# Kernel optimization log

Measured on AMD Instinct MI355X. Metric: run time of the kernel, lower is better.

## Reference

```python
import jax, jax.numpy as jnp
import numpy as np

B, S, D = 2, 2048, 2048
NH, NKV = 32, 8
HD = D // NH          # 64
NREP = NH // NKV      # 4


def _rope(x, cos, sin):
    # x: [B, S, H, HD]; cos/sin: [S, HD//2]
    x2 = x.reshape(*x.shape[:-1], HD // 2, 2)
    x0, x1 = x2[..., 0], x2[..., 1]
    c = cos[None, :, None, :]
    s = sin[None, :, None, :]
    r0 = x0 * c - x1 * s
    r1 = x0 * s + x1 * c
    return jnp.stack([r0, r1], axis=-1).reshape(x.shape)


def setup_inputs() -> dict:
    key = jax.random.key(0)
    ks = jax.random.split(key, 5)
    x = jax.random.normal(ks[0], (B, S, D), dtype=jnp.float32)
    wq = jax.random.normal(ks[1], (D, NH * HD), dtype=jnp.float32) * (D ** -0.5)
    wk = jax.random.normal(ks[2], (D, NKV * HD), dtype=jnp.float32) * (D ** -0.5)
    wv = jax.random.normal(ks[3], (D, NKV * HD), dtype=jnp.float32) * (D ** -0.5)
    wo = jax.random.normal(ks[4], (NH * HD, D), dtype=jnp.float32) * (D ** -0.5)
    # standard RoPE frequencies: theta = 10000^(-2i/HD)
    inv_freq = 1.0 / (10000.0 ** (np.arange(0, HD, 2, dtype=np.float32) / HD))
    angles = np.arange(S, dtype=np.float32)[:, None] * inv_freq[None, :]  # [S, HD/2]
    freqs_cos = jnp.asarray(np.cos(angles))
    freqs_sin = jnp.asarray(np.sin(angles))
    return {"x": x, "freqs_cos": freqs_cos, "freqs_sin": freqs_sin,
            "wq": wq, "wk": wk, "wv": wv, "wo": wo}


def reference(x, freqs_cos, freqs_sin, wq, wk, wv, wo):
    b, s, _ = x.shape
    xq = (x @ wq).reshape(b, s, NH, HD)
    xk = (x @ wk).reshape(b, s, NKV, HD)
    xv = (x @ wv).reshape(b, s, NKV, HD)
    xq = _rope(xq, freqs_cos, freqs_sin)
    xk = _rope(xk, freqs_cos, freqs_sin)
    # GQA repeat_kv: expand kv heads to NH
    keys = jnp.repeat(xk, NREP, axis=2)    # [B, S, NH, HD]
    values = jnp.repeat(xv, NREP, axis=2)
    scores = jnp.einsum('bqhd,bkhd->bhqk', xq, keys) / jnp.sqrt(jnp.float32(HD))
    causal = jnp.tril(jnp.ones((s, s), dtype=bool))
    scores = jnp.where(causal[None, None], scores, -jnp.inf)
    attn = jax.nn.softmax(scores.astype(jnp.float32), axis=-1).astype(xq.dtype)
    out = jnp.einsum('bhqk,bkhd->bqhd', attn, values).reshape(b, s, NH * HD)
    return out @ wo
```

## Files before the change

kernel.cpp:

```cpp
#include <hip/hip_runtime.h>
#include <hip/hip_bf16.h>

#define S_LEN 2048
#define DMODEL 2048
#define N_H 32
#define N_KV 8
#define H_D 64
#define ROWS 4096
#define QKV_LD 3072

typedef __bf16 bf16x8 __attribute__((ext_vector_type(8)));
typedef float f32x4 __attribute__((ext_vector_type(4)));

static __device__ __forceinline__ unsigned short f2bf(float f) {
  unsigned int u = __float_as_uint(f);
  u += 0x7FFFu + ((u >> 16) & 1u);
  return (unsigned short)(u >> 16);
}
static __device__ __forceinline__ unsigned short f2bf_tr(float f) {
  return (unsigned short)(__float_as_uint(f) >> 16);
}
static __device__ __forceinline__ float bf2f(unsigned short s) {
  return __uint_as_float((unsigned int)s << 16);
}

static __device__ __forceinline__ void async16(const void* g, void* l) {
  __builtin_amdgcn_global_load_lds(
      (const __attribute__((address_space(1))) unsigned int*)g,
      (__attribute__((address_space(3))) unsigned int*)l, 16, 0, 0);
}

__global__ __launch_bounds__(256) void cvt_bf16_k(
    const float* __restrict__ in, unsigned short* __restrict__ out) {
  const size_t i = ((size_t)blockIdx.x * 256 + threadIdx.x) * 8;
  const float4 a = *(const float4*)&in[i];
  const float4 b = *(const float4*)&in[i + 4];
  union { unsigned short u[8]; uint4 v; } p;
  p.u[0] = f2bf(a.x); p.u[1] = f2bf(a.y); p.u[2] = f2bf(a.z); p.u[3] = f2bf(a.w);
  p.u[4] = f2bf(b.x); p.u[5] = f2bf(b.y); p.u[6] = f2bf(b.z); p.u[7] = f2bf(b.w);
  *(uint4*)&out[i] = p.v;
}

__global__ __launch_bounds__(256) void prep_all_k(
    const float* __restrict__ x, const float* __restrict__ wq,
    const float* __restrict__ wk, const float* __restrict__ wv,
    const float* __restrict__ wo, unsigned short* __restrict__ xb,
    unsigned short* __restrict__ wqkvT, unsigned short* __restrict__ woT) {
  const int z = blockIdx.z;
  if (z == 4) {
    const size_t i =
        (((size_t)blockIdx.y * 64 + blockIdx.x) * 256 + threadIdx.x) * 8;
    const float4 a = *(const float4*)&x[i];
    const float4 b = *(const float4*)&x[i + 4];
    union { unsigned short u[8]; uint4 v; } p;
    p.u[0] = f2bf(a.x); p.u[1] = f2bf(a.y); p.u[2] = f2bf(a.z); p.u[3] = f2bf(a.w);
    p.u[4] = f2bf(b.x); p.u[5] = f2bf(b.y); p.u[6] = f2bf(b.z); p.u[7] = f2bf(b.w);
    *(uint4*)&xb[i] = p.v;
    return;
  }
  const float* in;
  unsigned short* out;
  int C;
  if (z == 0)      { in = wq; out = wqkvT;                  C = 2048; }
  else if (z == 1) { in = wk; out = wqkvT + 2048ull * 2048; C = 512;  }
  else if (z == 2) { in = wv; out = wqkvT + 2560ull * 2048; C = 512;  }
  else             { in = wo; out = woT;                    C = 2048; }
  if (blockIdx.x * 32 >= C) return;

  __shared__ unsigned short tile[32][33];
  const int tx = threadIdx.x & 31;
  const int ty = threadIdx.x >> 5;
  const int r0 = blockIdx.y * 32;
  const int c0 = blockIdx.x * 32;
#pragma unroll
  for (int i = 0; i < 32; i += 8)
    tile[ty + i][tx] = f2bf(in[(size_t)(r0 + ty + i) * C + c0 + tx]);
  __syncthreads();
#pragma unroll
  for (int i = 0; i < 32; i += 8)
    out[(size_t)(c0 + ty + i) * 2048 + r0 + tx] = tile[tx][ty + i];
}

#define SCALE_LOG2E 0.18033688011112042f

__global__ __launch_bounds__(256) void rope_vt_k(
    unsigned short* __restrict__ qkv, unsigned short* __restrict__ vT,
    const float* __restrict__ fc, const float* __restrict__ fs) {
  const int blk = blockIdx.x;
  if (blk < 20480) {
    const int PQ = ROWS * N_H * (H_D / 2);
    const int PK = ROWS * N_KV * (H_D / 2);
    const int idx = blk * 256 + threadIdx.x;
    if (idx >= PQ + PK) return;
    unsigned short* base;
    float c, sn;
    bool isq;
    if (idx < PQ) {
      const int i = idx & 31;
      const int h = (idx >> 5) & 31;
      const int row = idx >> 10;
      const int s = row & (S_LEN - 1);
      c = fc[s * 32 + i];
      sn = fs[s * 32 + i];
      base = qkv + (size_t)row * QKV_LD + h * H_D + 2 * i;
      isq = true;
    } else {
      const int p = idx - PQ;
      const int i = p & 31;
      const int h = (p >> 5) & 7;
      const int row = p >> 8;
      const int s = row & (S_LEN - 1);
      c = fc[s * 32 + i];
      sn = fs[s * 32 + i];
      base = qkv + (size_t)row * QKV_LD + 2048 + h * H_D + 2 * i;
      isq = false;
    }
    const float x0 = bf2f(base[0]);
    const float x1 = bf2f(base[1]);
    const float sc = isq ? SCALE_LOG2E : 1.0f;
    base[0] = f2bf((x0 * c - x1 * sn) * sc);
    base[1] = f2bf((x0 * sn + x1 * c) * sc);
  } else {
    __shared__ unsigned short tile[32][33];
    const int t = blk - 20480;
    const int bx = t & 15;
    const int by = t >> 4;
    const unsigned short* in = qkv + 2560;
    const int tx = threadIdx.x & 31;
    const int ty = threadIdx.x >> 5;
    const int r0 = by * 32;
    const int c0 = bx * 32;
#pragma unroll
    for (int i = 0; i < 32; i += 8)
      tile[ty + i][tx] = in[(size_t)(r0 + ty + i) * QKV_LD + c0 + tx];
    __syncthreads();
#pragma unroll
    for (int i = 0; i < 32; i += 8)
      vT[(size_t)(c0 + ty + i) * ROWS + r0 + tx] = tile[tx][ty + i];
  }
}

template <int STORE_BF16>
__global__ __launch_bounds__(256) void gemm_bt_k(
    const unsigned short* __restrict__ A, const unsigned short* __restrict__ BT,
    void* __restrict__ Cp, int M, int N, int K, int lda) {
  __shared__ __align__(16) unsigned short As[128 * 32];
  __shared__ __align__(16) unsigned short Bs[128 * 32];
  const int tid = threadIdx.x;
  const int wave = tid >> 6;
  const int lane = tid & 63;
  const int quad = lane >> 4;
  const int l16 = lane & 15;
  const int m0 = blockIdx.x * 128;
  const int n0 = blockIdx.y * 128;
  const int wm = (wave >> 1) * 64;
  const int wn = (wave & 1) * 64;
  const int rsub = lane >> 2;
  const int coff = (lane & 3) * 8;
  f32x4 acc[4][4] = {};

  for (int kt = 0; kt < K; kt += 32) {
    __syncthreads();
#pragma unroll
    for (int t = 0; t < 2; t++) {
      const int row = wave * 32 + t * 16 + rsub;
      async16(&A[(size_t)(m0 + row) * lda + kt + coff],
              &As[(wave * 32 + t * 16) * 32]);
      async16(&BT[(size_t)(n0 + row) * K + kt + coff],
              &Bs[(wave * 32 + t * 16) * 32]);
    }
    __syncthreads();
    bf16x8 af[4], bfr[4];
#pragma unroll
    for (int i = 0; i < 4; i++)
      af[i] = *(const bf16x8*)&As[(wm + i * 16 + l16) * 32 + quad * 8];
#pragma unroll
    for (int j = 0; j < 4; j++)
      bfr[j] = *(const bf16x8*)&Bs[(wn + j * 16 + l16) * 32 + quad * 8];
#pragma unroll
    for (int i = 0; i < 4; i++)
#pragma unroll
      for (int j = 0; j < 4; j++)
        acc[i][j] =
            __builtin_amdgcn_mfma_f32_16x16x32_bf16(af[i], bfr[j], acc[i][j], 0, 0, 0);
  }

#pragma unroll
  for (int i = 0; i < 4; i++) {
#pragma unroll
    for (int e = 0; e < 4; e++) {
      const int mrow = m0 + wm + i * 16 + quad * 4 + e;
#pragma unroll
      for (int j = 0; j < 4; j++) {
        const int ncol = n0 + wn + j * 16 + l16;
        const float val = acc[i][j][e];
        if (STORE_BF16) {
          ((unsigned short*)Cp)[(size_t)mrow * N + ncol] = f2bf(val);
        } else {
          ((float*)Cp)[(size_t)mrow * N + ncol] = val;
        }
      }
    }
  }
}

template <int AF32, int STORE_BF16>
__global__ __launch_bounds__(256) void gemm_k(
    const void* __restrict__ Ap, const float* __restrict__ B,
    void* __restrict__ Cp, int M, int N, int K) {
  constexpr int LDP = 40;
  __shared__ __align__(16) unsigned short As[128 * LDP];
  __shared__ __align__(16) unsigned short Bs[128 * LDP];
  const int tid = threadIdx.x;
  const int wave = tid >> 6;
  const int lane = tid & 63;
  const int quad = lane >> 4;
  const int l16 = lane & 15;
  const int m0 = blockIdx.x * 128;
  const int n0 = blockIdx.y * 128;
  const int wm = (wave >> 1) * 64;
  const int wn = (wave & 1) * 64;
  f32x4 acc[4][4] = {};

  for (int kt = 0; kt < K; kt += 32) {
    __syncthreads();
    if (AF32) {
      const float* A = (const float*)Ap;
      for (int c = tid; c < 1024; c += 256) {
        const int r = c >> 3;
        const int cc = (c & 7) << 2;
        const float4 w = *(const float4*)&A[(size_t)(m0 + r) * K + kt + cc];
        union { unsigned short u[4]; uint2 v; } p;
        p.u[0] = f2bf(w.x); p.u[1] = f2bf(w.y);
        p.u[2] = f2bf(w.z); p.u[3] = f2bf(w.w);
        *(uint2*)&As[r * LDP + cc] = p.v;
      }
    } else {
      const unsigned short* A = (const unsigned short*)Ap;
      for (int c = tid; c < 512; c += 256) {
        const int r = c >> 2;
        const int cc = (c & 3) << 3;
        *(uint4*)&As[r * LDP + cc] =
            *(const uint4*)&A[(size_t)(m0 + r) * K + kt + cc];
      }
    }
    for (int c = tid; c < 1024; c += 256) {
      const int kr = c >> 5;
      const int nc = (c & 31) << 2;
      const float4 w = *(const float4*)&B[(size_t)(kt + kr) * N + n0 + nc];
      Bs[(nc + 0) * LDP + kr] = f2bf(w.x);
      Bs[(nc + 1) * LDP + kr] = f2bf(w.y);
      Bs[(nc + 2) * LDP + kr] = f2bf(w.z);
      Bs[(nc + 3) * LDP + kr] = f2bf(w.w);
    }
    __syncthreads();
    bf16x8 af[4], bfr[4];
#pragma unroll
    for (int i = 0; i < 4; i++)
      af[i] = *(const bf16x8*)&As[(wm + i * 16 + l16) * LDP + quad * 8];
#pragma unroll
    for (int j = 0; j < 4; j++)
      bfr[j] = *(const bf16x8*)&Bs[(wn + j * 16 + l16) * LDP + quad * 8];
#pragma unroll
    for (int i = 0; i < 4; i++)
#pragma unroll
      for (int j = 0; j < 4; j++)
        acc[i][j] =
            __builtin_amdgcn_mfma_f32_16x16x32_bf16(af[i], bfr[j], acc[i][j], 0, 0, 0);
  }
#pragma unroll
  for (int i = 0; i < 4; i++) {
#pragma unroll
    for (int e = 0; e < 4; e++) {
      const int mrow = m0 + wm + i * 16 + quad * 4 + e;
#pragma unroll
      for (int j = 0; j < 4; j++) {
        const int ncol = n0 + wn + j * 16 + l16;
        const float val = acc[i][j][e];
        if (STORE_BF16) {
          ((unsigned short*)Cp)[(size_t)mrow * N + ncol] = f2bf(val);
        } else {
          ((float*)Cp)[(size_t)mrow * N + ncol] = val;
        }
      }
    }
  }
}

__global__ __launch_bounds__(256) void rope_k(
    unsigned short* __restrict__ q, unsigned short* __restrict__ kk,
    const float* __restrict__ fc, const float* __restrict__ fs,
    int qstride, int kstride) {
  const int PQ = ROWS * N_H * (H_D / 2);
  const int PK = ROWS * N_KV * (H_D / 2);
  const int idx = blockIdx.x * 256 + threadIdx.x;
  if (idx >= PQ + PK) return;
  unsigned short* base;
  float c, sn;
  if (idx < PQ) {
    const int i = idx & 31;
    const int h = (idx >> 5) & 31;
    const int row = idx >> 10;
    const int s = row & (S_LEN - 1);
    c = fc[s * 32 + i];
    sn = fs[s * 32 + i];
    base = q + (size_t)row * qstride + h * H_D + 2 * i;
  } else {
    const int p = idx - PQ;
    const int i = p & 31;
    const int h = (p >> 5) & 7;
    const int row = p >> 8;
    const int s = row & (S_LEN - 1);
    c = fc[s * 32 + i];
    sn = fs[s * 32 + i];
    base = kk + (size_t)row * kstride + h * H_D + 2 * i;
  }
  const float x0 = bf2f(base[0]);
  const float x1 = bf2f(base[1]);
  base[0] = f2bf(x0 * c - x1 * sn);
  base[1] = f2bf(x0 * sn + x1 * c);
}

#define LK 72

__global__ __launch_bounds__(256) void attn_mfma6_k(
    const unsigned short* __restrict__ qkv, const unsigned short* __restrict__ vT,
    unsigned short* __restrict__ ao) {
  const int pair = blockIdx.x, h = blockIdx.y, b = blockIdx.z;
  const int hk = h >> 2;
  const int tid = threadIdx.x;
  const int wave = tid >> 6;
  const int l16 = tid & 15;
  const int quad = (tid & 63) >> 4;
  const int rr = tid >> 2;
  const int dc = (tid & 3) * 16;

  __shared__ __align__(16) unsigned short Ks[2][64 * LK];
  __shared__ __align__(16) unsigned short Vt[2][64 * LK];
  __shared__ __align__(16) unsigned short Ps[4][32 * LK];

  bf16x8 ones;
#pragma unroll
  for (int j = 0; j < 8; j++) ones[j] = (__bf16)1.0f;

  const size_t kbase =
      (size_t)(b * S_LEN) * QKV_LD + 2048 + hk * H_D + dc;
  const size_t vbase = (size_t)(hk * H_D + rr) * ROWS + b * S_LEN + dc;

  for (int sel = 0; sel < 2; ++sel) {
    const int qb = sel ? (15 - pair) : pair;
    const int row0 = qb * 128;
    const int ktiles = 2 * qb + 2;

    bf16x8 af[2][2];
#pragma unroll
    for (int r = 0; r < 2; r++) {
      const size_t qrow =
          (size_t)(b * S_LEN + row0 + wave * 32 + r * 16 + l16);
#pragma unroll
      for (int c = 0; c < 2; c++)
        af[r][c] =
            *(const bf16x8*)&qkv[qrow * QKV_LD + h * H_D + c * 32 + quad * 8];
    }

    f32x4 o_acc[2][4] = {};
    f32x4 l_acc[2] = {};

    uint4 rk0, rk1, rv0, rv1;
    {
      const size_t kro = kbase + (size_t)rr * QKV_LD;
      rk0 = *(const uint4*)&qkv[kro];
      rk1 = *(const uint4*)&qkv[kro + 8];
      rv0 = *(const uint4*)&vT[vbase];
      rv1 = *(const uint4*)&vT[vbase + 8];
    }
    __syncthreads();
    *(uint4*)&Ks[0][rr * LK + dc] = rk0;
    *(uint4*)&Ks[0][rr * LK + dc + 8] = rk1;
    *(uint4*)&Vt[0][rr * LK + dc] = rv0;
    *(uint4*)&Vt[0][rr * LK + dc + 8] = rv1;

    int cur = 0;
    for (int kt = 0; kt < ktiles; ++kt) {
      if (kt + 1 < ktiles) {
        const size_t kro = kbase + (size_t)((kt + 1) * 64 + rr) * QKV_LD;
        rk0 = *(const uint4*)&qkv[kro];
        rk1 = *(const uint4*)&qkv[kro + 8];
        const size_t vro = vbase + (size_t)(kt + 1) * 64;
        rv0 = *(const uint4*)&vT[vro];
        rv1 = *(const uint4*)&vT[vro + 8];
      }
      __syncthreads();

      f32x4 sacc[2][4];
#pragma unroll
      for (int n = 0; n < 4; n++) {
        f32x4 z0 = {}, z1 = {};
#pragma unroll
        for (int c = 0; c < 2; c++) {
          const bf16x8 bk =
              *(const bf16x8*)&Ks[cur][(n * 16 + l16) * LK + c * 32 + quad * 8];
          z0 = __builtin_amdgcn_mfma_f32_16x16x32_bf16(af[0][c], bk, z0, 0, 0, 0);
          z1 = __builtin_amdgcn_mfma_f32_16x16x32_bf16(af[1][c], bk, z1, 0, 0, 0);
        }
        sacc[0][n] = z0;
        sacc[1][n] = z1;
      }

      const bool maybe_mask = (kt >= 2 * qb);
      const int krel0 = (kt - 2 * qb) * 64;
#pragma unroll
      for (int r = 0; r < 2; r++) {
        const int qrel = wave * 32 + r * 16 + quad * 4;
        if (maybe_mask) {
#pragma unroll
          for (int n = 0; n < 4; n++)
#pragma unroll
            for (int e = 0; e < 4; e++) {
              float pe = exp2f(sacc[r][n][e]);
              if ((krel0 + n * 16 + l16) > (qrel + e)) pe = 0.f;
              Ps[wave][(r * 16 + quad * 4 + e) * LK + n * 16 + l16] =
                  f2bf_tr(pe);
            }
        } else {
#pragma unroll
          for (int n = 0; n < 4; n++)
#pragma unroll
            for (int e = 0; e < 4; e++)
              Ps[wave][(r * 16 + quad * 4 + e) * LK + n * 16 + l16] =
                  f2bf_tr(exp2f(sacc[r][n][e]));
        }
      }

      bf16x8 pf[2][2];
#pragma unroll
      for (int r = 0; r < 2; r++)
#pragma unroll
        for (int c = 0; c < 2; c++)
          pf[r][c] = *(const bf16x8*)&Ps[wave][(r * 16 + l16) * LK + c * 32 +
                                              quad * 8];
#pragma unroll
      for (int c = 0; c < 2; c++) {
        l_acc[0] = __builtin_amdgcn_mfma_f32_16x16x32_bf16(pf[0][c], ones,
                                                           l_acc[0], 0, 0, 0);
        l_acc[1] = __builtin_amdgcn_mfma_f32_16x16x32_bf16(pf[1][c], ones,
                                                           l_acc[1], 0, 0, 0);
      }
#pragma unroll
      for (int n = 0; n < 4; n++)
#pragma unroll
        for (int c = 0; c < 2; c++) {
          const bf16x8 bv =
              *(const bf16x8*)&Vt[cur][(n * 16 + l16) * LK + c * 32 + quad * 8];
          o_acc[0][n] =
              __builtin_amdgcn_mfma_f32_16x16x32_bf16(pf[0][c], bv, o_acc[0][n], 0, 0, 0);
          o_acc[1][n] =
              __builtin_amdgcn_mfma_f32_16x16x32_bf16(pf[1][c], bv, o_acc[1][n], 0, 0, 0);
        }

      if (kt + 1 < ktiles) {
        const int nxt = cur ^ 1;
        *(uint4*)&Ks[nxt][rr * LK + dc] = rk0;
        *(uint4*)&Ks[nxt][rr * LK + dc + 8] = rk1;
        *(uint4*)&Vt[nxt][rr * LK + dc] = rv0;
        *(uint4*)&Vt[nxt][rr * LK + dc + 8] = rv1;
      }
      cur ^= 1;
    }

#pragma unroll
    for (int r = 0; r < 2; r++)
#pragma unroll
      for (int e = 0; e < 4; e++) {
        const float inv = 1.f / l_acc[r][e];
        const size_t row = (size_t)(b * S_LEN + row0 + wave * 32 + r * 16 +
                                    quad * 4 + e);
#pragma unroll
        for (int n = 0; n < 4; n++)
          ao[row * QKV_LD + h * H_D + n * 16 + l16] =
              f2bf(o_acc[r][n][e] * inv);
      }
  }
}

__global__ __launch_bounds__(256) void attn_mfma_k(
    const unsigned short* __restrict__ q, const unsigned short* __restrict__ k,
    const unsigned short* __restrict__ v, unsigned short* __restrict__ ao) {
  const int qt = blockIdx.x, h = blockIdx.y, b = blockIdx.z;
  const int hk = h >> 2;
  const int tid = threadIdx.x;
  const int wave = tid >> 6;
  const int l16 = tid & 15;
  const int quad = (tid & 63) >> 4;

  __shared__ __align__(16) unsigned short Ks[64 * LK];
  __shared__ __align__(16) unsigned short Vt[64 * LK];
  __shared__ __align__(16) unsigned short Ps[64 * LK];

  bf16x8 af[2];
  {
    const size_t qrow = (size_t)(b * S_LEN + qt * 64 + wave * 16 + l16);
#pragma unroll
    for (int c = 0; c < 2; c++)
      af[c] = *(const bf16x8*)&q[qrow * DMODEL + h * H_D + c * 32 + quad * 8];
  }

  f32x4 o_acc[4] = {};
  float m_i[4], l_i[4];
#pragma unroll
  for (int e = 0; e < 4; e++) { m_i[e] = -INFINITY; l_i[e] = 0.f; }

  for (int kt = 0; kt <= qt; ++kt) {
    const int kb = kt * 64;
    __syncthreads();
    {
      const int kr = tid >> 2;
      const int dc = (tid & 3) * 16;
      const size_t gro = (size_t)(b * S_LEN + kb + kr) * (N_KV * H_D) + hk * H_D + dc;
      *(uint4*)&Ks[kr * LK + dc] = *(const uint4*)&k[gro];
      *(uint4*)&Ks[kr * LK + dc + 8] = *(const uint4*)&k[gro + 8];
      union { unsigned short u[8]; uint4 v; } w0, w1;
      w0.v = *(const uint4*)&v[gro];
      w1.v = *(const uint4*)&v[gro + 8];
#pragma unroll
      for (int j = 0; j < 8; j++) Vt[(dc + j) * LK + kr] = w0.u[j];
#pragma unroll
      for (int j = 0; j < 8; j++) Vt[(dc + 8 + j) * LK + kr] = w1.u[j];
    }
    __syncthreads();

    f32x4 sacc[4];
#pragma unroll
    for (int n = 0; n < 4; n++) {
      f32x4 z = {};
#pragma unroll
      for (int c = 0; c < 2; c++) {
        const bf16x8 bk = *(const bf16x8*)&Ks[(n * 16 + l16) * LK + c * 32 + quad * 8];
        z = __builtin_amdgcn_mfma_f32_16x16x32_bf16(af[c], bk, z, 0, 0, 0);
      }
      sacc[n] = z;
    }

    float p[4][4], mnew[4];
#pragma unroll
    for (int e = 0; e < 4; e++) mnew[e] = m_i[e];
#pragma unroll
    for (int n = 0; n < 4; n++)
#pragma unroll
      for (int e = 0; e < 4; e++) {
        float s = sacc[n][e] * 0.125f;
        if (kt == qt && (n * 16 + l16) > (wave * 16 + quad * 4 + e))
          s = -INFINITY;
        p[n][e] = s;
        mnew[e] = fmaxf(mnew[e], s);
      }
#pragma unroll
    for (int e = 0; e < 4; e++) {
      mnew[e] = fmaxf(mnew[e], __shfl_xor(mnew[e], 1));
      mnew[e] = fmaxf(mnew[e], __shfl_xor(mnew[e], 2));
      mnew[e] = fmaxf(mnew[e], __shfl_xor(mnew[e], 4));
      mnew[e] = fmaxf(mnew[e], __shfl_xor(mnew[e], 8));
      const float alpha = __expf(m_i[e] - mnew[e]);
      m_i[e] = mnew[e];
      l_i[e] *= alpha;
#pragma unroll
      for (int n = 0; n < 4; n++) o_acc[n][e] *= alpha;
    }
#pragma unroll
    for (int n = 0; n < 4; n++)
#pragma unroll
      for (int e = 0; e < 4; e++) {
        const float pe = __expf(p[n][e] - m_i[e]);
        p[n][e] = pe;
        l_i[e] += pe;
      }

#pragma unroll
    for (int n = 0; n < 4; n++)
#pragma unroll
      for (int e = 0; e < 4; e++)
        Ps[(wave * 16 + quad * 4 + e) * LK + n * 16 + l16] = f2bf(p[n][e]);
    __syncthreads();

    bf16x8 pf[2];
#pragma unroll
    for (int c = 0; c < 2; c++)
      pf[c] = *(const bf16x8*)&Ps[(wave * 16 + l16) * LK + c * 32 + quad * 8];
#pragma unroll
    for (int n = 0; n < 4; n++)
#pragma unroll
      for (int c = 0; c < 2; c++) {
        const bf16x8 bv = *(const bf16x8*)&Vt[(n * 16 + l16) * LK + c * 32 + quad * 8];
        o_acc[n] = __builtin_amdgcn_mfma_f32_16x16x32_bf16(pf[c], bv, o_acc[n], 0, 0, 0);
      }
  }

#pragma unroll
  for (int e = 0; e < 4; e++) {
    l_i[e] += __shfl_xor(l_i[e], 1);
    l_i[e] += __shfl_xor(l_i[e], 2);
    l_i[e] += __shfl_xor(l_i[e], 4);
    l_i[e] += __shfl_xor(l_i[e], 8);
    const float inv = 1.f / l_i[e];
    const size_t row = (size_t)(b * S_LEN + qt * 64 + wave * 16 + quad * 4 + e);
#pragma unroll
    for (int n = 0; n < 4; n++)
      ao[row * DMODEL + h * H_D + n * 16 + l16] = f2bf(o_acc[n][e] * inv);
  }
}

extern "C" void kernel_launch(void* const* d_in, const int* in_sizes, int n_in,
                              void* d_out, int out_size, void* d_ws, size_t ws_size,
                              hipStream_t stream) {
  const float* x = (const float*)d_in[0];
  const float* fc = (const float*)d_in[1];
  const float* fs = (const float*)d_in[2];
  const float* wq = (const float*)d_in[3];
  const float* wk = (const float*)d_in[4];
  const float* wv = (const float*)d_in[5];
  const float* wo = (const float*)d_in[6];

  char* ws = (char*)d_ws;
  const dim3 b256(256);

  if (ws_size >= (64ull << 20)) {
    unsigned short* qkv = (unsigned short*)(ws);
    unsigned short* xb = (unsigned short*)(ws + (24ull << 20));
    unsigned short* wqkvT = (unsigned short*)(ws + (40ull << 20));
    unsigned short* woT = (unsigned short*)(ws + (52ull << 20));
    unsigned short* vT = (unsigned short*)(ws + (60ull << 20));

    prep_all_k<<<dim3(64, 64, 5), b256, 0, stream>>>(x, wq, wk, wv, wo, xb,
                                                     wqkvT, woT);

    gemm_bt_k<1><<<dim3(32, 24), b256, 0, stream>>>(xb, wqkvT, qkv, 4096, 3072,
                                                    2048, 2048);

    rope_vt_k<<<dim3(20480 + 2048), b256, 0, stream>>>(qkv, vT, fc, fs);

    attn_mfma6_k<<<dim3(8, N_H, 2), b256, 0, stream>>>(qkv, vT, qkv);

    gemm_bt_k<0><<<dim3(32, 16), b256, 0, stream>>>(qkv, woT, d_out, 4096, 2048,
                                                    2048, QKV_LD);
  } else {
    unsigned short* q = (unsigned short*)(ws);
    unsigned short* k = (unsigned short*)(ws + (16ull << 20));
    unsigned short* v = (unsigned short*)(ws + (20ull << 20));
    unsigned short* xb = (unsigned short*)(ws + (24ull << 20));
    const bool have_xb = ws_size >= (40ull << 20);

    if (have_xb) {
      cvt_bf16_k<<<dim3(ROWS * DMODEL / (256 * 8)), b256, 0, stream>>>(x, xb);
      gemm_k<0, 1><<<dim3(32, 16), b256, 0, stream>>>(xb, wq, q, 4096, 2048, 2048);
      gemm_k<0, 1><<<dim3(32, 4), b256, 0, stream>>>(xb, wk, k, 4096, 512, 2048);
      gemm_k<0, 1><<<dim3(32, 4), b256, 0, stream>>>(xb, wv, v, 4096, 512, 2048);
    } else {
      gemm_k<1, 1><<<dim3(32, 16), b256, 0, stream>>>(x, wq, q, 4096, 2048, 2048);
      gemm_k<1, 1><<<dim3(32, 4), b256, 0, stream>>>(x, wk, k, 4096, 512, 2048);
      gemm_k<1, 1><<<dim3(32, 4), b256, 0, stream>>>(x, wv, v, 4096, 512, 2048);
    }

    rope_k<<<dim3(20480), b256, 0, stream>>>(q, k, fc, fs, N_H * H_D, N_KV * H_D);
    attn_mfma_k<<<dim3(S_LEN / 64, N_H, 2), b256, 0, stream>>>(q, k, v, q);
    gemm_k<0, 0><<<dim3(32, 16), b256, 0, stream>>>(q, wo, d_out, 4096, 2048, 2048);
  }
}
```

Baseline: 331.1 us.

## Swizzle attention LDS tiles, swap QK MFMA operands, and launch one block per q-tile

The attention kernel drops padded LDS rows (stride 72) and uses XOR-swizzled 64-wide rows for K, V and P tiles to avoid bank conflicts while cutting shared memory. The QK^T MFMA operands are swapped so each lane holds four consecutive keys of one query row, which lets P be packed into a single 8-byte LDS store per fragment instead of scalar 2-byte stores. The paired causal q-block scheme (two q-tiles per block for load balance) is replaced by one q-tile per block with heaviest tiles first, doubling the grid. This trades the explicit balancing for more blocks, higher occupancy and less per-block serial work.

```diff
diff --git a/kernel.cpp b/kernel.cpp
--- a/kernel.cpp
+++ b/kernel.cpp
@@ -16,9 +16,6 @@
   unsigned int u = __float_as_uint(f);
   u += 0x7FFFu + ((u >> 16) & 1u);
   return (unsigned short)(u >> 16);
-}
-static __device__ __forceinline__ unsigned short f2bf_tr(float f) {
-  return (unsigned short)(__float_as_uint(f) >> 16);
 }
 static __device__ __forceinline__ float bf2f(unsigned short s) {
   return __uint_as_float((unsigned int)s << 16);
@@ -321,12 +318,11 @@
   base[1] = f2bf(x0 * sn + x1 * c);
 }
 
-#define LK 72
-
-__global__ __launch_bounds__(256) void attn_mfma6_k(
+__global__ __launch_bounds__(256) void attn_mfma7_k(
     const unsigned short* __restrict__ qkv, const unsigned short* __restrict__ vT,
     unsigned short* __restrict__ ao) {
-  const int pair = blockIdx.x, h = blockIdx.y, b = blockIdx.z;
+  const int qb = 15 - blockIdx.x;
+  const int h = blockIdx.y, b = blockIdx.z;
   const int hk = h >> 2;
   const int tid = threadIdx.x;
   const int wave = tid >> 6;
@@ -334,154 +330,152 @@
   const int quad = (tid & 63) >> 4;
   const int rr = tid >> 2;
   const int dc = (tid & 3) * 16;
-
-  __shared__ __align__(16) unsigned short Ks[2][64 * LK];
-  __shared__ __align__(16) unsigned short Vt[2][64 * LK];
-  __shared__ __align__(16) unsigned short Ps[4][32 * LK];
+  const int rx = (l16 & 7) << 3;
+  const int sx = (rr & 7) << 3;
+
+  __shared__ __align__(16) unsigned short Ks[2][64 * 64];
+  __shared__ __align__(16) unsigned short Vt[2][64 * 64];
+  __shared__ __align__(16) unsigned short Ps[4][32 * 64];
 
   bf16x8 ones;
 #pragma unroll
   for (int j = 0; j < 8; j++) ones[j] = (__bf16)1.0f;
+
+  const int row0 = qb * 128;
+  const int ktiles = 2 * qb + 2;
+
+  bf16x8 af[2][2];
+#pragma unroll
+  for (int r = 0; r < 2; r++) {
+    const size_t qrow = (size_t)(b * S_LEN + row0 + wave * 32 + r * 16 + l16);
+#pragma unroll
+    for (int c = 0; c < 2; c++)
+      af[r][c] =
+          *(const bf16x8*)&qkv[qrow * QKV_LD + h * H_D + c * 32 + quad * 8];
+  }
+
+  f32x4 o_acc[2][4] = {};
+  f32x4 l_acc[2] = {};
 
   const size_t kbase =
       (size_t)(b * S_LEN) * QKV_LD + 2048 + hk * H_D + dc;
   const size_t vbase = (size_t)(hk * H_D + rr) * ROWS + b * S_LEN + dc;
 
-  for (int sel = 0; sel < 2; ++sel) {
-    const int qb = sel ? (15 - pair) : pair;
-    const int row0 = qb * 128;
-    const int ktiles = 2 * qb + 2;
-
-    bf16x8 af[2][2];
-#pragma unroll
-    for (int r = 0; r < 2; r++) {
-      const size_t qrow =
-          (size_t)(b * S_LEN + row0 + wave * 32 + r * 16 + l16);
-#pragma unroll
-      for (int c = 0; c < 2; c++)
-        af[r][c] =
-            *(const bf16x8*)&qkv[qrow * QKV_LD + h * H_D + c * 32 + quad * 8];
-    }
-
-    f32x4 o_acc[2][4] = {};
-    f32x4 l_acc[2] = {};
-
-    uint4 rk0, rk1, rv0, rv1;
-    {
-      const size_t kro = kbase + (size_t)rr * QKV_LD;
+  uint4 rk0, rk1, rv0, rv1;
+  {
+    const size_t kro = kbase + (size_t)rr * QKV_LD;
+    rk0 = *(const uint4*)&qkv[kro];
+    rk1 = *(const uint4*)&qkv[kro + 8];
+    rv0 = *(const uint4*)&vT[vbase];
+    rv1 = *(const uint4*)&vT[vbase + 8];
+  }
+  *(uint4*)&Ks[0][rr * 64 + (dc ^ sx)] = rk0;
+  *(uint4*)&Ks[0][rr * 64 + ((dc + 8) ^ sx)] = rk1;
+  *(uint4*)&Vt[0][rr * 64 + (dc ^ sx)] = rv0;
+  *(uint4*)&Vt[0][rr * 64 + ((dc + 8) ^ sx)] = rv1;
+
+  int cur = 0;
+  for (int kt = 0; kt < ktiles; ++kt) {
+    if (kt + 1 < ktiles) {
+      const size_t kro = kbase + (size_t)((kt + 1) * 64 + rr) * QKV_LD;
       rk0 = *(const uint4*)&qkv[kro];
       rk1 = *(const uint4*)&qkv[kro + 8];
-      rv0 = *(const uint4*)&vT[vbase];
-      rv1 = *(const uint4*)&vT[vbase + 8];
-    }
-    __syncthreads();
-    *(uint4*)&Ks[0][rr * LK + dc] = rk0;
-    *(uint4*)&Ks[0][rr * LK + dc + 8] = rk1;
-    *(uint4*)&Vt[0][rr * LK + dc] = rv0;
-    *(uint4*)&Vt[0][rr * LK + dc + 8] = rv1;
-
-    int cur = 0;
-    for (int kt = 0; kt < ktiles; ++kt) {
-      if (kt + 1 < ktiles) {
-        const size_t kro = kbase + (size_t)((kt + 1) * 64 + rr) * QKV_LD;
-        rk0 = *(const uint4*)&qkv[kro];
-        rk1 = *(const uint4*)&qkv[kro + 8];
-        const size_t vro = vbase + (size_t)(kt + 1) * 64;
-        rv0 = *(const uint4*)&vT[vro];
-        rv1 = *(const uint4*)&vT[vro + 8];
-      }
-      __syncthreads();
-
-      f32x4 sacc[2][4];
+      const size_t vro = vbase + (size_t)(kt + 1) * 64;
+      rv0 = *(const uint4*)&vT[vro];
+      rv1 = *(const uint4*)&vT[vro + 8];
+    }
+    __syncthreads();
+
+    f32x4 sacc[2][4];
+#pragma unroll
+    for (int n = 0; n < 4; n++) {
+      f32x4 z0 = {}, z1 = {};
+#pragma unroll
+      for (int c = 0; c < 2; c++) {
+        const bf16x8 bk = *(const bf16x8*)&Ks[cur][(n * 16 + l16) * 64 +
+                                                   ((c * 32 + quad * 8) ^ rx)];
+        z0 = __builtin_amdgcn_mfma_f32_16x16x32_bf16(bk, af[0][c], z0, 0, 0, 0);
+        z1 = __builtin_amdgcn_mfma_f32_16x16x32_bf16(bk, af[1][c], z1, 0, 0, 0);
+      }
+      sacc[0][n] = z0;
+      sacc[1][n] = z1;
+    }
+
+    const bool maybe_mask = (kt >= 2 * qb);
+    const int krel0 = (kt - 2 * qb) * 64;
+#pragma unroll
+    for (int r = 0; r < 2; r++) {
+      const int qn = wave * 32 + r * 16 + l16;
+      const int prow = (r * 16 + l16) * 64;
 #pragma unroll
       for (int n = 0; n < 4; n++) {
-        f32x4 z0 = {}, z1 = {};
-#pragma unroll
-        for (int c = 0; c < 2; c++) {
-          const bf16x8 bk =
-              *(const bf16x8*)&Ks[cur][(n * 16 + l16) * LK + c * 32 + quad * 8];
-          z0 = __builtin_amdgcn_mfma_f32_16x16x32_bf16(af[0][c], bk, z0, 0, 0, 0);
-          z1 = __builtin_amdgcn_mfma_f32_16x16x32_bf16(af[1][c], bk, z1, 0, 0, 0);
+        const int kb0 = krel0 + n * 16 + quad * 4;
+        float pe[4];
+#pragma unroll
+        for (int e = 0; e < 4; e++) {
+          float v = exp2f(sacc[r][n][e]);
+          if (maybe_mask && (kb0 + e > qn)) v = 0.f;
+          pe[e] = v;
         }
-        sacc[0][n] = z0;
-        sacc[1][n] = z1;
-      }
-
-      const bool maybe_mask = (kt >= 2 * qb);
-      const int krel0 = (kt - 2 * qb) * 64;
-#pragma unroll
-      for (int r = 0; r < 2; r++) {
-        const int qrel = wave * 32 + r * 16 + quad * 4;
-        if (maybe_mask) {
-#pragma unroll
-          for (int n = 0; n < 4; n++)
-#pragma unroll
-            for (int e = 0; e < 4; e++) {
-              float pe = exp2f(sacc[r][n][e]);
-              if ((krel0 + n * 16 + l16) > (qrel + e)) pe = 0.f;
-              Ps[wave][(r * 16 + quad * 4 + e) * LK + n * 16 + l16] =
-                  f2bf_tr(pe);
-            }
-        } else {
-#pragma unroll
-          for (int n = 0; n < 4; n++)
-#pragma unroll
-            for (int e = 0; e < 4; e++)
-              Ps[wave][(r * 16 + quad * 4 + e) * LK + n * 16 + l16] =
-                  f2bf_tr(exp2f(sacc[r][n][e]));
-        }
-      }
-
-      bf16x8 pf[2][2];
-#pragma unroll
-      for (int r = 0; r < 2; r++)
-#pragma unroll
-        for (int c = 0; c < 2; c++)
-          pf[r][c] = *(const bf16x8*)&Ps[wave][(r * 16 + l16) * LK + c * 32 +
-                                              quad * 8];
+        uint2 u;
+        u.x = (__float_as_uint(pe[0]) >> 16) |
+              (__float_as_uint(pe[1]) & 0xFFFF0000u);
+        u.y = (__float_as_uint(pe[2]) >> 16) |
+              (__float_as_uint(pe[3]) & 0xFFFF0000u);
+        *(uint2*)&Ps[wave][prow + ((n * 16 + quad * 4) ^ rx)] = u;
+      }
+    }
+
+    bf16x8 pf[2][2];
+#pragma unroll
+    for (int r = 0; r < 2; r++)
+#pragma unroll
+      for (int c = 0; c < 2; c++)
+        pf[r][c] = *(const bf16x8*)&Ps[wave][(r * 16 + l16) * 64 +
+                                            ((c * 32 + quad * 8) ^ rx)];
+#pragma unroll
+    for (int c = 0; c < 2; c++) {
+      l_acc[0] = __builtin_amdgcn_mfma_f32_16x16x32_bf16(pf[0][c], ones,
+                                                         l_acc[0], 0, 0, 0);
+      l_acc[1] = __builtin_amdgcn_mfma_f32_16x16x32_bf16(pf[1][c], ones,
+                                                         l_acc[1], 0, 0, 0);
+    }
+#pragma unroll
+    for (int n = 0; n < 4; n++)
 #pragma unroll
       for (int c = 0; c < 2; c++) {
-        l_acc[0] = __builtin_amdgcn_mfma_f32_16x16x32_bf16(pf[0][c], ones,
-                                                           l_acc[0], 0, 0, 0);
-        l_acc[1] = __builtin_amdgcn_mfma_f32_16x16x32_bf16(pf[1][c], ones,
-                                                           l_acc[1], 0, 0, 0);
-      }
+        const bf16x8 bv = *(const bf16x8*)&Vt[cur][(n * 16 + l16) * 64 +
+                                                   ((c * 32 + quad * 8) ^ rx)];
+        o_acc[0][n] = __builtin_amdgcn_mfma_f32_16x16x32_bf16(pf[0][c], bv,
+                                                              o_acc[0][n], 0, 0, 0);
+        o_acc[1][n] = __builtin_amdgcn_mfma_f32_16x16x32_bf16(pf[1][c], bv,
+                                                              o_acc[1][n], 0, 0, 0);
+      }
+
+    if (kt + 1 < ktiles) {
+      const int nxt = cur ^ 1;
+      *(uint4*)&Ks[nxt][rr * 64 + (dc ^ sx)] = rk0;
+      *(uint4*)&Ks[nxt][rr * 64 + ((dc + 8) ^ sx)] = rk1;
+      *(uint4*)&Vt[nxt][rr * 64 + (dc ^ sx)] = rv0;
+      *(uint4*)&Vt[nxt][rr * 64 + ((dc + 8) ^ sx)] = rv1;
+    }
+    cur ^= 1;
+  }
+
+#pragma unroll
+  for (int r = 0; r < 2; r++)
+#pragma unroll
+    for (int e = 0; e < 4; e++) {
+      const float inv = 1.f / l_acc[r][e];
+      const size_t row =
+          (size_t)(b * S_LEN + row0 + wave * 32 + r * 16 + quad * 4 + e);
 #pragma unroll
       for (int n = 0; n < 4; n++)
-#pragma unroll
-        for (int c = 0; c < 2; c++) {
-          const bf16x8 bv =
-              *(const bf16x8*)&Vt[cur][(n * 16 + l16) * LK + c * 32 + quad * 8];
-          o_acc[0][n] =
-              __builtin_amdgcn_mfma_f32_16x16x32_bf16(pf[0][c], bv, o_acc[0][n], 0, 0, 0);
-          o_acc[1][n] =
-              __builtin_amdgcn_mfma_f32_16x16x32_bf16(pf[1][c], bv, o_acc[1][n], 0, 0, 0);
-        }
-
-      if (kt + 1 < ktiles) {
-        const int nxt = cur ^ 1;
-        *(uint4*)&Ks[nxt][rr * LK + dc] = rk0;
-        *(uint4*)&Ks[nxt][rr * LK + dc + 8] = rk1;
-        *(uint4*)&Vt[nxt][rr * LK + dc] = rv0;
-        *(uint4*)&Vt[nxt][rr * LK + dc + 8] = rv1;
-      }
-      cur ^= 1;
-    }
-
-#pragma unroll
-    for (int r = 0; r < 2; r++)
-#pragma unroll
-      for (int e = 0; e < 4; e++) {
-        const float inv = 1.f / l_acc[r][e];
-        const size_t row = (size_t)(b * S_LEN + row0 + wave * 32 + r * 16 +
-                                    quad * 4 + e);
-#pragma unroll
-        for (int n = 0; n < 4; n++)
-          ao[row * QKV_LD + h * H_D + n * 16 + l16] =
-              f2bf(o_acc[r][n][e] * inv);
-      }
-  }
-}
+        ao[row * QKV_LD + h * H_D + n * 16 + l16] = f2bf(o_acc[r][n][e] * inv);
+    }
+}
+
+#define LK 72
 
 __global__ __launch_bounds__(256) void attn_mfma_k(
     const unsigned short* __restrict__ q, const unsigned short* __restrict__ k,
@@ -638,7 +632,7 @@
 
     rope_vt_k<<<dim3(20480 + 2048), b256, 0, stream>>>(qkv, vT, fc, fs);
 
-    attn_mfma6_k<<<dim3(8, N_H, 2), b256, 0, stream>>>(qkv, vT, qkv);
+    attn_mfma7_k<<<dim3(16, N_H, 2), b256, 0, stream>>>(qkv, vT, qkv);
 
     gemm_bt_k<0><<<dim3(32, 16), b256, 0, stream>>>(qkv, woT, d_out, 4096, 2048,
                                                     2048, QKV_LD);
```

Result: slower. 400.3 us (+20.9%).
